# Performance work log

Hardware: AMD Instinct MI355X
Metric: run time of the kernel (lower is better)

The kernel has to match this reference:

```python
import jax, jax.numpy as jnp
import numpy as np
import math

B, T, C, F = 8, 2048, 1024, 4096
N_LAYER, LAYER_ID = 12, 1


def _init_params(key):
    ks = jax.random.split(key, 16)
    s = 0.02
    ratio_0_to_1 = LAYER_ID / (N_LAYER - 1)
    ratio_1_to_almost0 = 1.0 - LAYER_ID / N_LAYER
    h = np.arange(C, dtype=np.float32)
    decay = -5.0 + 8.0 * (h / (C - 1)) ** (0.7 + 1.3 * ratio_0_to_1)
    zigzag = np.array([((i + 1) % 3 - 1) for i in range(C)], dtype=np.float32) * 0.5
    first = np.ones(C, dtype=np.float32) * math.log(0.3) + zigzag
    xi = (np.arange(C, dtype=np.float32) / C)
    p = {
        'ln1_w': jnp.ones(C), 'ln1_b': jnp.zeros(C),
        'ln2_w': jnp.ones(C), 'ln2_b': jnp.zeros(C),
        'att_time_decay': jnp.asarray(decay),
        'att_time_first': jnp.asarray(first),
        'att_mix_k': jnp.asarray(xi ** ratio_1_to_almost0),
        'att_mix_v': jnp.asarray(xi ** ratio_1_to_almost0 + 0.3 * ratio_0_to_1),
        'att_mix_r': jnp.asarray(xi ** (0.5 * ratio_1_to_almost0)),
        'att_Wk': jax.random.normal(ks[0], (C, C)) * s,
        'att_Wv': jax.random.normal(ks[1], (C, C)) * s,
        'att_Wr': jax.random.normal(ks[2], (C, C)) * s,
        'att_Wo': jax.random.normal(ks[3], (C, C)) * s,
        'ffn_mix_k': jnp.asarray(xi ** ratio_1_to_almost0),
        'ffn_mix_r': jnp.asarray(xi ** ratio_1_to_almost0),
        'ffn_Wk': jax.random.normal(ks[4], (F, C)) * s,
        'ffn_Wr': jax.random.normal(ks[5], (C, C)) * s,
        'ffn_Wv': jax.random.normal(ks[6], (C, F)) * s,
        'short_W': jax.random.normal(ks[7], (C, C)) * s,
    }
    return p


def setup_inputs() -> dict:
    key = jax.random.key(0)
    k1, k2 = jax.random.split(key)
    inp = {'x': jax.random.normal(k1, (B, T, C), dtype=jnp.float32)}
    inp.update(_init_params(k2))
    return inp


def _layernorm(x, w, b, eps=1e-5):
    mu = jnp.mean(x, axis=-1, keepdims=True)
    var = jnp.var(x, axis=-1, keepdims=True)
    return (x - mu) * jax.lax.rsqrt(var + eps) * w + b


def _time_shift(x):
    # ZeroPad2d((0,0,1,-1)): prepend zero row along T, drop last
    return jnp.pad(x, ((0, 0), (1, 0), (0, 0)))[:, :-1]


def _wkv(time_decay, time_first, k, v):
    # numerically-stable WKV recurrence, matching the CUDA kernel math
    w = -jnp.exp(time_decay)  # [C]
    u = time_first            # [C]
    kt = jnp.swapaxes(k, 0, 1)  # [T,B,C]
    vt = jnp.swapaxes(v, 0, 1)
    a0 = jnp.zeros(k.shape[::2] if False else (k.shape[0], k.shape[2]), k.dtype)
    b0 = jnp.zeros_like(a0)
    p0 = jnp.full_like(a0, -1e30)

    def step(carry, kv):
        a, b, p = carry
        k_t, v_t = kv
        ww = u + k_t
        q = jnp.maximum(p, ww)
        e1 = jnp.exp(p - q)
        e2 = jnp.exp(ww - q)
        y = (e1 * a + e2 * v_t) / (e1 * b + e2)
        ww2 = p + w
        q2 = jnp.maximum(ww2, k_t)
        f1 = jnp.exp(ww2 - q2)
        f2 = jnp.exp(k_t - q2)
        return (f1 * a + f2 * v_t, f1 * b + f2, q2), y

    _, ys = jax.lax.scan(step, (a0, b0, p0), (kt, vt))
    return jnp.swapaxes(ys, 0, 1)  # [B,T,C]


def _lin(x, W):
    return jnp.einsum('btc,oc->bto', x, W)


def reference(x, ln1_w, ln1_b, ln2_w, ln2_b,
              att_time_decay, att_time_first, att_mix_k, att_mix_v, att_mix_r,
              att_Wk, att_Wv, att_Wr, att_Wo,
              ffn_mix_k, ffn_mix_r, ffn_Wk, ffn_Wr, ffn_Wv, short_W):
    # --- TimeMix on ln1(x) ---
    h = _layernorm(x, ln1_w, ln1_b)
    hh = _time_shift(h)
    xk = h * att_mix_k + hh * (1 - att_mix_k)
    xv = h * att_mix_v + hh * (1 - att_mix_v)
    xr = h * att_mix_r + hh * (1 - att_mix_r)
    k = _lin(xk, att_Wk)
    v = _lin(xv, att_Wv)
    sr = jax.nn.sigmoid(_lin(xr, att_Wr))
    rwkv = sr * _wkv(att_time_decay, att_time_first, k, v)
    att_out = _lin(rwkv, att_Wo)
    # shortcut linear replaces identity residual (L3TC Block)
    x = _lin(x, short_W) + att_out
    # --- ChannelMix on ln2(x) ---
    g = _layernorm(x, ln2_w, ln2_b)
    gg = _time_shift(g)
    gk = g * ffn_mix_k + gg * (1 - ffn_mix_k)
    gr = g * ffn_mix_r + gg * (1 - ffn_mix_r)
    kk = jnp.square(jax.nn.relu(_lin(gk, ffn_Wk)))
    kv = _lin(kk, ffn_Wv)
    rkv = jax.nn.sigmoid(_lin(gr, ffn_Wr)) * kv
    return x + rkv
```

## Files before the change

kernel.cpp:

```cpp
#include <hip/hip_runtime.h>

#define BB 8
#define TT 2048
#define CC 1024
#define FF 4096
#define MM (BB*TT)

typedef unsigned short u16;
typedef __bf16 bf16x8 __attribute__((ext_vector_type(8)));
typedef float f32x4 __attribute__((ext_vector_type(4)));

__device__ __forceinline__ u16 f2bf(float f) {
  unsigned int u = __float_as_uint(f);
  u += 0x7fffu + ((u >> 16) & 1u);
  return (u16)(u >> 16);
}
__device__ __forceinline__ float bf2f(u16 h) {
  unsigned int u = ((unsigned int)h) << 16;
  return __uint_as_float(u);
}
__device__ __forceinline__ float sigm(float x) { return 1.f / (1.f + __expf(-x)); }

__device__ __forceinline__ void async16(const void* g, void* l) {
  __builtin_amdgcn_global_load_lds(
      (const __attribute__((address_space(1))) unsigned int*)g,
      (__attribute__((address_space(3))) unsigned int*)l, 16, 0, 0);
}

#define GROUP_M 16

#define DSR(d, a) asm volatile("ds_read_b128 %0, %1" : "=v"(d) : "v"(a))
#define MFMA16(A_, B_, C_) \
  (C_) = __builtin_amdgcn_mfma_f32_16x16x32_bf16( \
      __builtin_bit_cast(bf16x8, (A_)), __builtin_bit_cast(bf16x8, (B_)), (C_), 0, 0, 0)

#define PH_MID() do { \
  __builtin_amdgcn_s_barrier(); \
  asm volatile("s_waitcnt lgkmcnt(0)"); \
  __builtin_amdgcn_sched_barrier(0); \
  __builtin_amdgcn_s_setprio(1); } while (0)

#define PH_END() do { \
  __builtin_amdgcn_s_setprio(0); \
  __builtin_amdgcn_sched_barrier(0); \
  __builtin_amdgcn_s_barrier(); } while (0)

template<int MODE>
__global__ __launch_bounds__(512, 2) void gemm_bt(
    const u16* __restrict__ A, const u16* __restrict__ W,
    float* __restrict__ Cf, u16* __restrict__ Cb,
    const u16* __restrict__ R, int N, int K)
{
  __shared__ __align__(16) u16 ldsA[2][256 * 64];
  __shared__ __align__(16) u16 ldsB[2][256 * 64];

  const int tid  = threadIdx.x;
  const int wave = tid >> 6;
  const int lane = tid & 63;
  const int wmi  = wave >> 2;
  const int wni  = wave & 3;
  const int lm   = lane & 15;
  const int lq   = lane >> 4;

  const int bid  = blockIdx.x + blockIdx.y * gridDim.x;
  const int gsz  = GROUP_M * gridDim.y;
  const int gid  = bid / gsz;
  const int rem  = bid - gid * gsz;
  const int bm   = (gid * GROUP_M + (rem % GROUP_M)) * 256;
  const int bn   = (rem / GROUP_M) * 256;

  const int NT = K >> 6;

  const int srow   = wave * 8 + (lane >> 3);
  const int schunk = (lane & 7) ^ (lane >> 3);
  const u16* gA = A + (size_t)(bm + srow) * K + schunk * 8;
  const u16* gB = W + (size_t)(bn + srow) * K + schunk * 8;
  const size_t rowK = (size_t)64 * K;

  auto stA = [&](int buf, int q, int t2) {
    async16(gA + (size_t)t2 * 64 + (size_t)q * rowK,
            &ldsA[buf][(q * 64 + wave * 8) * 64]);
  };
  auto stB = [&](int buf, int q, int t2) {
    async16(gB + (size_t)t2 * 64 + (size_t)q * rowK,
            &ldsB[buf][(q * 64 + wave * 8) * 64]);
  };

  const unsigned lAbase =
      (unsigned)(size_t)(const __attribute__((address_space(3))) u16*)&ldsA[0][0];
  const unsigned lBbase =
      (unsigned)(size_t)(const __attribute__((address_space(3))) u16*)&ldsB[0][0];
  const unsigned aof0 = (unsigned)((wmi * 128 + lm) * 128 + (((lq    ) ^ (lm & 7)) * 16));
  const unsigned aof1 = (unsigned)((wmi * 128 + lm) * 128 + (((lq + 4) ^ (lm & 7)) * 16));
  const unsigned bof0 = (unsigned)((wni *  64 + lm) * 128 + (((lq    ) ^ (lm & 7)) * 16));
  const unsigned bof1 = (unsigned)((wni *  64 + lm) * 128 + (((lq + 4) ^ (lm & 7)) * 16));

  f32x4 acc[8][4] = {};
  f32x4 a0[4][2], a1[4][2], b[2][2];

  stA(0, 0, 0); stA(0, 1, 0); stA(0, 2, 0); stA(0, 3, 0);
  stB(0, 0, 0); stB(0, 1, 0); stB(0, 2, 0); stB(0, 3, 0);
  stA(1, 0, 1); stA(1, 2, 1); stA(1, 1, 1); stA(1, 3, 1);
  stB(1, 0, 1); stB(1, 1, 1);
  asm volatile("s_waitcnt vmcnt(4)");
  __builtin_amdgcn_s_barrier();
#pragma unroll
  for (int mi = 0; mi < 4; ++mi) {
    DSR(a0[mi][0], lAbase + aof0 + mi * 2048);
    DSR(a0[mi][1], lAbase + aof1 + mi * 2048);
  }

  for (int t = 0; t < NT; ++t) {
    const int cur = t & 1, nxt = cur ^ 1;
    const unsigned cA = lAbase + cur * 32768;
    const unsigned cB = lBbase + cur * 32768;
    const unsigned nA = lAbase + nxt * 32768;
    const bool s2 = (t + 2 < NT);
    const bool s1 = (t + 1 < NT);

#pragma unroll
    for (int ni = 0; ni < 2; ++ni) {
      DSR(b[ni][0], cB + bof0 + ni * 2048);
      DSR(b[ni][1], cB + bof1 + ni * 2048);
    }
    if (s2) { stA(cur, 0, t + 2); stA(cur, 2, t + 2); }
    if (s1) { stB(nxt, 2, t + 1); stB(nxt, 3, t + 1); }
    PH_MID();
#pragma unroll
    for (int mi = 0; mi < 4; ++mi)
#pragma unroll
      for (int ni = 0; ni < 2; ++ni) {
        MFMA16(a0[mi][0], b[ni][0], acc[mi][ni]);
        MFMA16(a0[mi][1], b[ni][1], acc[mi][ni]);
      }
    PH_END();

#pragma unroll
    for (int mi = 0; mi < 4; ++mi) {
      DSR(a1[mi][0], cA + aof0 + (4 + mi) * 2048);
      DSR(a1[mi][1], cA + aof1 + (4 + mi) * 2048);
    }
    PH_MID();
#pragma unroll
    for (int mi = 0; mi < 4; ++mi)
#pragma unroll
      for (int ni = 0; ni < 2; ++ni) {
        MFMA16(a1[mi][0], b[ni][0], acc[4 + mi][ni]);
        MFMA16(a1[mi][1], b[ni][1], acc[4 + mi][ni]);
      }
    PH_END();

#pragma unroll
    for (int ni = 0; ni < 2; ++ni) {
      DSR(b[ni][0], cB + bof0 + (2 + ni) * 2048);
      DSR(b[ni][1], cB + bof1 + (2 + ni) * 2048);
    }
    if (s2) { stA(cur, 1, t + 2); stA(cur, 3, t + 2); }
    PH_MID();
#pragma unroll
    for (int mi = 0; mi < 4; ++mi)
#pragma unroll
      for (int ni = 0; ni < 2; ++ni) {
        MFMA16(a0[mi][0], b[ni][0], acc[mi][2 + ni]);
        MFMA16(a0[mi][1], b[ni][1], acc[mi][2 + ni]);
      }
    PH_END();

    if (s1) {
#pragma unroll
      for (int mi = 0; mi < 4; ++mi) {
        DSR(a0[mi][0], nA + aof0 + mi * 2048);
        DSR(a0[mi][1], nA + aof1 + mi * 2048);
      }
    }
    if (s2) { stB(cur, 0, t + 2); stB(cur, 1, t + 2); }
    PH_MID();
#pragma unroll
    for (int mi = 0; mi < 4; ++mi)
#pragma unroll
      for (int ni = 0; ni < 2; ++ni) {
        MFMA16(a1[mi][0], b[ni][0], acc[4 + mi][2 + ni]);
        MFMA16(a1[mi][1], b[ni][1], acc[4 + mi][2 + ni]);
      }
    __builtin_amdgcn_s_setprio(0);
    __builtin_amdgcn_sched_barrier(0);
    if (t < NT - 2) asm volatile("s_waitcnt vmcnt(4)");
    else            asm volatile("s_waitcnt vmcnt(0)");
    __builtin_amdgcn_s_barrier();
  }

  const int row0 = bm + wmi * 128 + lq * 4;
  const int col0 = bn + wni * 64 + lm;
#pragma unroll
  for (int mi = 0; mi < 8; ++mi)
#pragma unroll
    for (int ni = 0; ni < 4; ++ni) {
      size_t base = (size_t)(row0 + mi * 16) * N + (col0 + ni * 16);
#pragma unroll
      for (int r2 = 0; r2 < 4; ++r2) {
        size_t idx = base + (size_t)r2 * N;
        float v = acc[mi][ni][r2];
        if (MODE == 0) Cf[idx] = v;
        if (MODE == 2) { float rl = v > 0.f ? v : 0.f; Cb[idx] = f2bf(rl * rl); }
        if (MODE == 3) Cb[idx] = f2bf(v);
        if (MODE == 4) Cf[idx] += sigm(bf2f(R[idx])) * v;
      }
    }
}

__global__ __launch_bounds__(256) void prep_mix(
    const float* __restrict__ x,
    const float* __restrict__ lnw, const float* __restrict__ lnb,
    const float* __restrict__ mk, const float* __restrict__ mv, const float* __restrict__ mr,
    u16* __restrict__ ok, u16* __restrict__ ov, u16* __restrict__ orr,
    u16* __restrict__ oxb)
{
  const int m = blockIdx.x;
  const int t = m & (TT - 1);
  const int tid = threadIdx.x;
  const int wave = tid >> 6, lane = tid & 63;
  const bool hasp = (t != 0);

  const float4 xc4 = ((const float4*)(x + (size_t)m * CC))[tid];
  float4 xp4 = make_float4(0.f, 0.f, 0.f, 0.f);
  if (hasp) xp4 = ((const float4*)(x + (size_t)(m - 1) * CC))[tid];

  float s0 = xc4.x + xc4.y + xc4.z + xc4.w;
  float s1 = xc4.x*xc4.x + xc4.y*xc4.y + xc4.z*xc4.z + xc4.w*xc4.w;
  float s2 = xp4.x + xp4.y + xp4.z + xp4.w;
  float s3 = xp4.x*xp4.x + xp4.y*xp4.y + xp4.z*xp4.z + xp4.w*xp4.w;
#pragma unroll
  for (int off2 = 32; off2 > 0; off2 >>= 1) {
    s0 += __shfl_xor(s0, off2);
    s1 += __shfl_xor(s1, off2);
    s2 += __shfl_xor(s2, off2);
    s3 += __shfl_xor(s3, off2);
  }
  __shared__ float red[4][4];
  if (lane == 0) { red[0][wave] = s0; red[1][wave] = s1; red[2][wave] = s2; red[3][wave] = s3; }
  __syncthreads();
  const float S0 = red[0][0] + red[0][1] + red[0][2] + red[0][3];
  const float S1 = red[1][0] + red[1][1] + red[1][2] + red[1][3];
  const float S2 = red[2][0] + red[2][1] + red[2][2] + red[2][3];
  const float S3 = red[3][0] + red[3][1] + red[3][2] + red[3][3];
  const float inv = 1.f / (float)CC;
  const float muc = S0 * inv, varc = S1 * inv - muc * muc, rsc = rsqrtf(varc + 1e-5f);
  const float mup = S2 * inv, varp = S3 * inv - mup * mup, rsp = rsqrtf(varp + 1e-5f);

  const float xc[4] = {xc4.x, xc4.y, xc4.z, xc4.w};
  const float xp[4] = {xp4.x, xp4.y, xp4.z, xp4.w};
  const float4 lw4 = ((const float4*)lnw)[tid];
  const float4 lb4 = ((const float4*)lnb)[tid];
  const float lw[4] = {lw4.x, lw4.y, lw4.z, lw4.w};
  const float lb[4] = {lb4.x, lb4.y, lb4.z, lb4.w};
  const float4 mk4 = ((const float4*)mk)[tid];
  const float mka[4] = {mk4.x, mk4.y, mk4.z, mk4.w};
  const float4 mr4 = ((const float4*)mr)[tid];
  const float mra[4] = {mr4.x, mr4.y, mr4.z, mr4.w};
  float mva[4] = {0.f, 0.f, 0.f, 0.f};
  if (ov) {
    const float4 mv4 = ((const float4*)mv)[tid];
    mva[0] = mv4.x; mva[1] = mv4.y; mva[2] = mv4.z; mva[3] = mv4.w;
  }

  ushort4 wk2, wv2, wr2, wb2;
  u16* pk = (u16*)&wk2; u16* pv = (u16*)&wv2; u16* pr = (u16*)&wr2; u16* pb = (u16*)&wb2;
#pragma unroll
  for (int j = 0; j < 4; ++j) {
    float h  = (xc[j] - muc) * rsc * lw[j] + lb[j];
    float hh = hasp ? (xp[j] - mup) * rsp * lw[j] + lb[j] : 0.f;
    pk[j] = f2bf(h * mka[j] + hh * (1.f - mka[j]));
    pv[j] = f2bf(h * mva[j] + hh * (1.f - mva[j]));
    pr[j] = f2bf(h * mra[j] + hh * (1.f - mra[j]));
    pb[j] = f2bf(xc[j]);
  }
  ((ushort4*)(ok + (size_t)m * CC))[tid] = wk2;
  if (ov)  ((ushort4*)(ov  + (size_t)m * CC))[tid] = wv2;
  ((ushort4*)(orr + (size_t)m * CC))[tid] = wr2;
  if (oxb) ((ushort4*)(oxb + (size_t)m * (2 * CC)))[tid] = wb2;
}

#define WKV_CPB 32
#define WKV_NCH 32
#define WKV_L   (TT / WKV_NCH)

__global__ __launch_bounds__(1024) void wkv_scan(
    const u16* __restrict__ k, const u16* __restrict__ v, const u16* __restrict__ r,
    const float* __restrict__ decay, const float* __restrict__ first,
    u16* __restrict__ out)
{
  const int b  = blockIdx.x >> 5;
  const int c0 = (blockIdx.x & 31) * WKV_CPB;
  const int tid = threadIdx.x;
  const int cl = tid & 31;
  const int j  = tid >> 5;
  const int c  = c0 + cl;

  const float w   = -__expf(decay[c]);
  const float lam = __expf(w);
  const float eu  = __expf(first[c]);

  const size_t base  = (size_t)b * TT * CC + (size_t)j * WKV_L * CC + c;
  size_t obase = ((size_t)b * TT + (size_t)j * WKV_L) * (2 * CC) + c;

  float a = 0.f, bb = 0.f;
  size_t idx = base;
  for (int i = 0; i < WKV_L; ++i, idx += CC) {
    const float kt = bf2f(k[idx]), vt = bf2f(v[idx]);
    const float ek = __expf(kt);
    a  = fmaf(lam, a, ek * vt);
    bb = fmaf(lam, bb, ek);
  }

  __shared__ float sA[WKV_NCH][WKV_CPB];
  __shared__ float sB[WKV_NCH][WKV_CPB];
  sA[j][cl] = a; sB[j][cl] = bb;
  __syncthreads();
  if (tid < WKV_CPB) {
    float ca = 0.f, cb = 0.f;
    const float cw   = -__expf(decay[c0 + tid]);
    const float cLam = __expf(cw * (float)WKV_L);
#pragma unroll
    for (int q = 0; q < WKV_NCH; ++q) {
      const float ta = sA[q][tid], tb = sB[q][tid];
      sA[q][tid] = ca; sB[q][tid] = cb;
      ca = fmaf(cLam, ca, ta);
      cb = fmaf(cLam, cb, tb);
    }
  }
  __syncthreads();
  a = sA[j][cl]; bb = sB[j][cl];

  idx = base;
  for (int i = 0; i < WKV_L; ++i, idx += CC, obase += 2 * CC) {
    const float kt = bf2f(k[idx]), vt = bf2f(v[idx]), rt = bf2f(r[idx]);
    const float ek = __expf(kt);
    const float e2 = eu * ek;
    const float y  = (a + e2 * vt) / (bb + e2);
    out[obase] = f2bf(sigm(rt) * y);
    a  = fmaf(lam, a, ek * vt);
    bb = fmaf(lam, bb, ek);
  }
}

struct ConvArgs { const float* src[8]; int end[8]; int dstoff[8]; };

__global__ __launch_bounds__(256) void conv_w(ConvArgs args, u16* __restrict__ dst)
{
  const int i = (blockIdx.x * 256 + threadIdx.x) * 4;
  int seg = 0;
  const float* sp = args.src[0];
  int base = 0;
#pragma unroll
  for (int s = 1; s < 8; ++s) {
    if (i >= args.end[s - 1]) { seg = s; sp = args.src[s]; base = args.end[s - 1]; }
  }
  const int l = i - base;
  const float4 vv = *(const float4*)(sp + l);
  int dsti;
  if (seg == 3)      { int row = l >> 10, col = l & 1023; dsti = args.dstoff[3] + row * 2048 + 1024 + col; }
  else if (seg == 4) { int row = l >> 10, col = l & 1023; dsti = args.dstoff[4] + row * 2048 + col; }
  else               dsti = args.dstoff[seg] + l;
  ushort4 d;
  d.x = f2bf(vv.x); d.y = f2bf(vv.y); d.z = f2bf(vv.z); d.w = f2bf(vv.w);
  *(ushort4*)(dst + dsti) = d;
}

extern "C" void kernel_launch(void* const* d_in, const int* in_sizes, int n_in,
                              void* d_out, int out_size, void* d_ws, size_t ws_size,
                              hipStream_t stream)
{
  const float* x    = (const float*)d_in[0];
  const float* ln1w = (const float*)d_in[1];
  const float* ln1b = (const float*)d_in[2];
  const float* ln2w = (const float*)d_in[3];
  const float* ln2b = (const float*)d_in[4];
  const float* tdec = (const float*)d_in[5];
  const float* tfir = (const float*)d_in[6];
  const float* amk  = (const float*)d_in[7];
  const float* amv  = (const float*)d_in[8];
  const float* amr  = (const float*)d_in[9];
  const float* Wk   = (const float*)d_in[10];
  const float* Wv   = (const float*)d_in[11];
  const float* Wr   = (const float*)d_in[12];
  const float* Wo   = (const float*)d_in[13];
  const float* fmk  = (const float*)d_in[14];
  const float* fmr  = (const float*)d_in[15];
  const float* WfK  = (const float*)d_in[16];
  const float* WfR  = (const float*)d_in[17];
  const float* WfV  = (const float*)d_in[18];
  const float* Wsh  = (const float*)d_in[19];
  float* out = (float*)d_out;
  char* ws = (char*)d_ws;

  u16* wW = (u16*)(ws);
  u16* U0 = (u16*)(ws + 29360128);
  u16* U1 = (u16*)(ws + 62914560);
  u16* U2 = (u16*)(ws + 96468992);
  u16* U3 = (u16*)(ws + 130023424);
  u16* U4 = (u16*)(ws + 163577856);

  u16* xk   = U0;
  u16* xv   = U1;
  u16* xr   = U2;
  u16* Ap   = U4;
  u16* kbuf = U3;
  u16* vbuf = U0;
  u16* rbuf = U1;
  u16* gk   = U0;
  u16* gr   = U1;
  u16* kkb  = U2;
  u16* rffn = U0;

  u16* bWk   = wW + 0;
  u16* bWv   = wW + 1048576;
  u16* bWr   = wW + 2097152;
  u16* bWsWo = wW + 3145728;
  u16* bWfR  = wW + 5242880;
  u16* bWfK  = wW + 6291456;
  u16* bWfV  = wW + 10485760;

  ConvArgs ca;
  ca.src[0] = Wk;  ca.src[1] = Wv;  ca.src[2] = Wr;  ca.src[3] = Wo;
  ca.src[4] = Wsh; ca.src[5] = WfR; ca.src[6] = WfK; ca.src[7] = WfV;
  const int e = 1048576;
  ca.end[0] = e;     ca.end[1] = 2*e;  ca.end[2] = 3*e;  ca.end[3] = 4*e;
  ca.end[4] = 5*e;   ca.end[5] = 6*e;  ca.end[6] = 10*e; ca.end[7] = 14*e;
  ca.dstoff[0] = 0;     ca.dstoff[1] = e;    ca.dstoff[2] = 2*e;
  ca.dstoff[3] = 3*e;   ca.dstoff[4] = 3*e;
  ca.dstoff[5] = 5*e;   ca.dstoff[6] = 6*e;  ca.dstoff[7] = 10*e;

  conv_w<<<14336, 256, 0, stream>>>(ca, wW);
  prep_mix<<<MM, 256, 0, stream>>>(x, ln1w, ln1b, amk, amv, amr, xk, xv, xr, Ap);

  dim3 g8(MM / 256, CC / 256);
  gemm_bt<3><<<g8, 512, 0, stream>>>(xk, bWk, nullptr, kbuf, nullptr, CC, CC);
  gemm_bt<3><<<g8, 512, 0, stream>>>(xv, bWv, nullptr, vbuf, nullptr, CC, CC);
  gemm_bt<3><<<g8, 512, 0, stream>>>(xr, bWr, nullptr, rbuf, nullptr, CC, CC);

  wkv_scan<<<BB * (CC / WKV_CPB), 1024, 0, stream>>>(kbuf, vbuf, rbuf, tdec, tfir, Ap + CC);

  gemm_bt<0><<<g8, 512, 0, stream>>>(Ap, bWsWo, out, nullptr, nullptr, CC, 2 * CC);

  prep_mix<<<MM, 256, 0, stream>>>(out, ln2w, ln2b, fmk, nullptr, fmr, gk, nullptr, gr, nullptr);

  dim3 gF(MM / 256, FF / 256);
  gemm_bt<2><<<gF, 512, 0, stream>>>(gk, bWfK, nullptr, kkb, nullptr, FF, CC);
  gemm_bt<3><<<g8, 512, 0, stream>>>(gr, bWfR, nullptr, rffn, nullptr, CC, CC);
  gemm_bt<4><<<g8, 512, 0, stream>>>(kkb, bWfV, out, nullptr, rffn, CC, FF);
}
```

Baseline: 836.5 us.

## Restructure GEMM main loop into two-tile unrolled pipeline with immediate-offset LDS reads

Replaces the per-iteration software pipeline with a macro-based schedule that unrolls two K-tiles per loop. It uses immediate offsets on ds_read_b128, separate B register banks, and barriers only after the waits. Global staging now writes the buffer just consumed, two tiles ahead, with a new B row permutation and LDS read layout. The aim is to cut address arithmetic and barrier stalls and to overlap loads better with MFMA. The risks are a different vmcnt gating pattern that may expose memory latency, and more registers.

```diff
diff --git a/kernel.cpp b/kernel.cpp
--- a/kernel.cpp
+++ b/kernel.cpp
@@ -29,21 +29,71 @@
 
 #define GROUP_M 16
 
-#define DSR(d, a) asm volatile("ds_read_b128 %0, %1" : "=v"(d) : "v"(a))
+#define DSRD(d, a, o) \
+  asm volatile("ds_read_b128 %0, %1 offset:%c2" : "=v"(d) : "v"(a), "i"(o))
+
 #define MFMA16(A_, B_, C_) \
   (C_) = __builtin_amdgcn_mfma_f32_16x16x32_bf16( \
       __builtin_bit_cast(bf16x8, (A_)), __builtin_bit_cast(bf16x8, (B_)), (C_), 0, 0, 0)
 
-#define PH_MID() do { \
-  __builtin_amdgcn_s_barrier(); \
-  asm volatile("s_waitcnt lgkmcnt(0)"); \
+#define READ_A(bank, BETA, MB) do { \
+  DSRD(bank[0][0], aAddr0, (BETA)*32768 + ((MB)+0)*2048); \
+  DSRD(bank[0][1], aAddr1, (BETA)*32768 + ((MB)+0)*2048); \
+  DSRD(bank[1][0], aAddr0, (BETA)*32768 + ((MB)+1)*2048); \
+  DSRD(bank[1][1], aAddr1, (BETA)*32768 + ((MB)+1)*2048); \
+  DSRD(bank[2][0], aAddr0, (BETA)*32768 + ((MB)+2)*2048); \
+  DSRD(bank[2][1], aAddr1, (BETA)*32768 + ((MB)+2)*2048); \
+  DSRD(bank[3][0], aAddr0, (BETA)*32768 + ((MB)+3)*2048); \
+  DSRD(bank[3][1], aAddr1, (BETA)*32768 + ((MB)+3)*2048); \
+} while (0)
+
+#define READ_B(bank, BETA, NB) do { \
+  DSRD(bank[0][0], bAddr0, (BETA)*32768 + (((NB)+0)>>1)*16384 + (((NB)+0)&1)*2048); \
+  DSRD(bank[0][1], bAddr1, (BETA)*32768 + (((NB)+0)>>1)*16384 + (((NB)+0)&1)*2048); \
+  DSRD(bank[1][0], bAddr0, (BETA)*32768 + (((NB)+1)>>1)*16384 + (((NB)+1)&1)*2048); \
+  DSRD(bank[1][1], bAddr1, (BETA)*32768 + (((NB)+1)>>1)*16384 + (((NB)+1)&1)*2048); \
+} while (0)
+
+#define QMFMA(ABANK, BBANK, AO, NO) do { \
+  _Pragma("unroll") \
+  for (int mi = 0; mi < 4; ++mi) \
+    _Pragma("unroll") \
+    for (int ni = 0; ni < 2; ++ni) { \
+      MFMA16(ABANK[mi][0], BBANK[ni][0], acc[(AO)+mi][(NO)+ni]); \
+      MFMA16(ABANK[mi][1], BBANK[ni][1], acc[(AO)+mi][(NO)+ni]); \
+    } \
+} while (0)
+
+#define PH_EXEC_BEGIN() do { \
   __builtin_amdgcn_sched_barrier(0); \
   __builtin_amdgcn_s_setprio(1); } while (0)
 
-#define PH_END() do { \
+#define PH_EXEC_END(GATE) do { \
   __builtin_amdgcn_s_setprio(0); \
   __builtin_amdgcn_sched_barrier(0); \
-  __builtin_amdgcn_s_barrier(); } while (0)
+  asm volatile("s_waitcnt lgkmcnt(0)"); \
+  if (GATE) asm volatile("s_waitcnt vmcnt(0)"); \
+  __builtin_amdgcn_s_barrier(); \
+  __builtin_amdgcn_sched_barrier(0); } while (0)
+
+#define TILE(T2A, BETA, DOSTAGE, RDQ2, RDQ3) do { \
+   \
+  READ_A(a1, BETA, 4); \
+  PH_EXEC_BEGIN(); QMFMA(a0, b01, 0, 0); PH_EXEC_END(0); \
+   \
+  READ_B(b23, BETA, 2); \
+  PH_EXEC_BEGIN(); QMFMA(a1, b01, 4, 0); PH_EXEC_END(1); \
+   \
+  if (RDQ2) READ_B(b01, (BETA)^1, 0); \
+  if (DOSTAGE) { stA(BETA, 0, T2A); stA(BETA, 1, T2A); \
+                 stB(BETA, 0, T2A); stB(BETA, 1, T2A); } \
+  PH_EXEC_BEGIN(); QMFMA(a0, b23, 0, 2); PH_EXEC_END(0); \
+   \
+  if (RDQ3) READ_A(a0, (BETA)^1, 0); \
+  if (DOSTAGE) { stA(BETA, 2, T2A); stA(BETA, 3, T2A); \
+                 stB(BETA, 2, T2A); stB(BETA, 3, T2A); } \
+  PH_EXEC_BEGIN(); QMFMA(a1, b23, 4, 2); PH_EXEC_END(0); \
+} while (0)
 
 template<int MODE>
 __global__ __launch_bounds__(512, 2) void gemm_bt(
@@ -71,10 +121,12 @@
 
   const int NT = K >> 6;
 
-  const int srow   = wave * 8 + (lane >> 3);
-  const int schunk = (lane & 7) ^ (lane >> 3);
-  const u16* gA = A + (size_t)(bm + srow) * K + schunk * 8;
-  const u16* gB = W + (size_t)(bn + srow) * K + schunk * 8;
+  const int ls     = lane >> 3;
+  const int schunk = (lane & 7) ^ ls;
+  const int rowA   = wave * 8 + ls;
+  const int rowB   = (wave >> 2) * 64 + (wave & 3) * 8 + ls;
+  const u16* gA = A + (size_t)(bm + rowA) * K + schunk * 8;
+  const u16* gB = W + (size_t)(bn + rowB) * K + schunk * 8;
   const size_t rowK = (size_t)64 * K;
 
   auto stA = [&](int buf, int q, int t2) {
@@ -82,7 +134,8 @@
             &ldsA[buf][(q * 64 + wave * 8) * 64]);
   };
   auto stB = [&](int buf, int q, int t2) {
-    async16(gB + (size_t)t2 * 64 + (size_t)q * rowK,
+    const int qrow = (q == 0) ? 0 : (q == 1) ? 128 : (q == 2) ? 32 : 160;
+    async16(gB + (size_t)t2 * 64 + (size_t)qrow * K,
             &ldsB[buf][(q * 64 + wave * 8) * 64]);
   };
 
@@ -90,104 +143,33 @@
       (unsigned)(size_t)(const __attribute__((address_space(3))) u16*)&ldsA[0][0];
   const unsigned lBbase =
       (unsigned)(size_t)(const __attribute__((address_space(3))) u16*)&ldsB[0][0];
-  const unsigned aof0 = (unsigned)((wmi * 128 + lm) * 128 + (((lq    ) ^ (lm & 7)) * 16));
-  const unsigned aof1 = (unsigned)((wmi * 128 + lm) * 128 + (((lq + 4) ^ (lm & 7)) * 16));
-  const unsigned bof0 = (unsigned)((wni *  64 + lm) * 128 + (((lq    ) ^ (lm & 7)) * 16));
-  const unsigned bof1 = (unsigned)((wni *  64 + lm) * 128 + (((lq + 4) ^ (lm & 7)) * 16));
+  const unsigned aAddr0 = lAbase + (unsigned)((wmi * 128 + lm) * 128 + (((lq    ) ^ (lm & 7)) * 16));
+  const unsigned aAddr1 = lAbase + (unsigned)((wmi * 128 + lm) * 128 + (((lq + 4) ^ (lm & 7)) * 16));
+  const unsigned bAddr0 = lBbase + (unsigned)((wni * 32 + lm) * 128 + (((lq    ) ^ (lm & 7)) * 16));
+  const unsigned bAddr1 = lBbase + (unsigned)((wni * 32 + lm) * 128 + (((lq + 4) ^ (lm & 7)) * 16));
 
   f32x4 acc[8][4] = {};
-  f32x4 a0[4][2], a1[4][2], b[2][2];
+  f32x4 a0[4][2], a1[4][2], b01[2][2], b23[2][2];
 
   stA(0, 0, 0); stA(0, 1, 0); stA(0, 2, 0); stA(0, 3, 0);
   stB(0, 0, 0); stB(0, 1, 0); stB(0, 2, 0); stB(0, 3, 0);
-  stA(1, 0, 1); stA(1, 2, 1); stA(1, 1, 1); stA(1, 3, 1);
-  stB(1, 0, 1); stB(1, 1, 1);
-  asm volatile("s_waitcnt vmcnt(4)");
+  stA(1, 0, 1); stA(1, 1, 1); stA(1, 2, 1); stA(1, 3, 1);
+  stB(1, 0, 1); stB(1, 1, 1); stB(1, 2, 1); stB(1, 3, 1);
+  asm volatile("s_waitcnt vmcnt(0)");
   __builtin_amdgcn_s_barrier();
-#pragma unroll
-  for (int mi = 0; mi < 4; ++mi) {
-    DSR(a0[mi][0], lAbase + aof0 + mi * 2048);
-    DSR(a0[mi][1], lAbase + aof1 + mi * 2048);
-  }
-
-  for (int t = 0; t < NT; ++t) {
-    const int cur = t & 1, nxt = cur ^ 1;
-    const unsigned cA = lAbase + cur * 32768;
-    const unsigned cB = lBbase + cur * 32768;
-    const unsigned nA = lAbase + nxt * 32768;
-    const bool s2 = (t + 2 < NT);
-    const bool s1 = (t + 1 < NT);
-
-#pragma unroll
-    for (int ni = 0; ni < 2; ++ni) {
-      DSR(b[ni][0], cB + bof0 + ni * 2048);
-      DSR(b[ni][1], cB + bof1 + ni * 2048);
-    }
-    if (s2) { stA(cur, 0, t + 2); stA(cur, 2, t + 2); }
-    if (s1) { stB(nxt, 2, t + 1); stB(nxt, 3, t + 1); }
-    PH_MID();
-#pragma unroll
-    for (int mi = 0; mi < 4; ++mi)
-#pragma unroll
-      for (int ni = 0; ni < 2; ++ni) {
-        MFMA16(a0[mi][0], b[ni][0], acc[mi][ni]);
-        MFMA16(a0[mi][1], b[ni][1], acc[mi][ni]);
-      }
-    PH_END();
-
-#pragma unroll
-    for (int mi = 0; mi < 4; ++mi) {
-      DSR(a1[mi][0], cA + aof0 + (4 + mi) * 2048);
-      DSR(a1[mi][1], cA + aof1 + (4 + mi) * 2048);
-    }
-    PH_MID();
-#pragma unroll
-    for (int mi = 0; mi < 4; ++mi)
-#pragma unroll
-      for (int ni = 0; ni < 2; ++ni) {
-        MFMA16(a1[mi][0], b[ni][0], acc[4 + mi][ni]);
-        MFMA16(a1[mi][1], b[ni][1], acc[4 + mi][ni]);
-      }
-    PH_END();
-
-#pragma unroll
-    for (int ni = 0; ni < 2; ++ni) {
-      DSR(b[ni][0], cB + bof0 + (2 + ni) * 2048);
-      DSR(b[ni][1], cB + bof1 + (2 + ni) * 2048);
-    }
-    if (s2) { stA(cur, 1, t + 2); stA(cur, 3, t + 2); }
-    PH_MID();
-#pragma unroll
-    for (int mi = 0; mi < 4; ++mi)
-#pragma unroll
-      for (int ni = 0; ni < 2; ++ni) {
-        MFMA16(a0[mi][0], b[ni][0], acc[mi][2 + ni]);
-        MFMA16(a0[mi][1], b[ni][1], acc[mi][2 + ni]);
-      }
-    PH_END();
-
-    if (s1) {
-#pragma unroll
-      for (int mi = 0; mi < 4; ++mi) {
-        DSR(a0[mi][0], nA + aof0 + mi * 2048);
-        DSR(a0[mi][1], nA + aof1 + mi * 2048);
-      }
-    }
-    if (s2) { stB(cur, 0, t + 2); stB(cur, 1, t + 2); }
-    PH_MID();
-#pragma unroll
-    for (int mi = 0; mi < 4; ++mi)
-#pragma unroll
-      for (int ni = 0; ni < 2; ++ni) {
-        MFMA16(a1[mi][0], b[ni][0], acc[4 + mi][2 + ni]);
-        MFMA16(a1[mi][1], b[ni][1], acc[4 + mi][2 + ni]);
-      }
-    __builtin_amdgcn_s_setprio(0);
-    __builtin_amdgcn_sched_barrier(0);
-    if (t < NT - 2) asm volatile("s_waitcnt vmcnt(4)");
-    else            asm volatile("s_waitcnt vmcnt(0)");
-    __builtin_amdgcn_s_barrier();
-  }
+  READ_A(a0, 0, 0);
+  READ_B(b01, 0, 0);
+  asm volatile("s_waitcnt lgkmcnt(0)");
+  __builtin_amdgcn_sched_barrier(0);
+  __builtin_amdgcn_s_barrier();
+
+  for (int t = 0; t + 3 < NT; t += 2) {
+    TILE(t + 2, 0, 1, 1, 1);
+    TILE(t + 3, 1, 1, 1, 1);
+  }
+
+  TILE(0, 0, 0, 1, 1);
+  TILE(0, 1, 0, 0, 0);
 
   const int row0 = bm + wmi * 128 + lq * 4;
   const int col0 = bn + wni * 64 + lm;
```

Result: slower. 1.817 ms (+117.2%).
